# Optimization experiments

Hardware: AMD Instinct MI355X
Metric: run time of the kernel (lower is better)

The kernel has to match this reference:

```python
import jax, jax.numpy as jnp
import numpy as np

B, D_IN, D_LAT, K = 8192, 768, 12288, 64


def setup_inputs() -> dict:
    key = jax.random.key(0)
    k1, k2, k3 = jax.random.split(key, 3)
    x = jax.random.normal(k1, (B, D_IN), dtype=jnp.float32)
    # Kaiming-uniform-ish init scale (matches nn.Linear default magnitude)
    W_enc = jax.random.normal(k2, (D_IN, D_LAT), dtype=jnp.float32) * (1.0 / np.sqrt(D_IN))
    b_enc = jnp.zeros((D_LAT,), dtype=jnp.float32)
    W_dec = jax.random.normal(k3, (D_LAT, D_IN), dtype=jnp.float32) * (1.0 / np.sqrt(D_LAT))
    b_dec = jnp.zeros((D_IN,), dtype=jnp.float32)
    return {"x": x, "W_enc": W_enc, "b_enc": b_enc, "W_dec": W_dec, "b_dec": b_dec, "k_top": K}


def topk_activation(h, k):
    # keep top-k values per row, zero the rest (equivalent to zeros_like + scatter_)
    if k >= h.shape[1]:
        return h
    vals, idx = jax.lax.top_k(h, k)                  # [B, k]
    rows = jnp.arange(h.shape[0])[:, None]           # [B, 1]
    return jnp.zeros_like(h).at[rows, idx].set(vals)


def reference(x, W_enc, b_enc, W_dec, b_dec, k_top):
    h = x @ W_enc + b_enc                            # [B, D_LAT]
    z = topk_activation(h, k_top)                    # sparse latent [B, D_LAT]
    recon = z @ W_dec + b_dec                        # [B, D_IN]
    return recon, z
```

## Files before the change

### kernel.cpp

```cpp
#include <hip/hip_runtime.h>
#include <stdint.h>

#define BROWS 8192
#define DIN   768
#define DLAT  12288
#define KTOP  64

#define LO_SCALE 4096.0f
#define LO_INV   (1.0f / 4096.0f)


typedef _Float16 half8 __attribute__((ext_vector_type(8)));
typedef __attribute__((ext_vector_type(4))) float float4v;

typedef __attribute__((address_space(3))) void lds_void_t;
typedef __attribute__((address_space(1))) void glob_void_t;

__device__ __forceinline__ unsigned short f2h_bits(float f) {
  _Float16 h = (_Float16)f;
  return __builtin_bit_cast(unsigned short, h);
}
__device__ __forceinline__ float h_bits_to_f(unsigned short b) {
  return (float)__builtin_bit_cast(_Float16, b);
}

__global__ __launch_bounds__(256) void k_cvt_split(const float* __restrict__ in,
                                                   unsigned short* __restrict__ hi,
                                                   unsigned short* __restrict__ lo,
                                                   int n4) {
  int i = blockIdx.x * 256 + threadIdx.x;
  if (i >= n4) return;
  float4 v = ((const float4*)in)[i];
  ushort4 h, l;
  h.x = f2h_bits(v.x); l.x = f2h_bits((v.x - h_bits_to_f(h.x)) * LO_SCALE);
  h.y = f2h_bits(v.y); l.y = f2h_bits((v.y - h_bits_to_f(h.y)) * LO_SCALE);
  h.z = f2h_bits(v.z); l.z = f2h_bits((v.z - h_bits_to_f(h.z)) * LO_SCALE);
  h.w = f2h_bits(v.w); l.w = f2h_bits((v.w - h_bits_to_f(h.w)) * LO_SCALE);
  ((ushort4*)hi)[i] = h;
  ((ushort4*)lo)[i] = l;
}

__global__ __launch_bounds__(256) void k_transpose_split(const float* __restrict__ W,
                                                         unsigned short* __restrict__ Wth,
                                                         unsigned short* __restrict__ Wtl) {
  __shared__ float s[32][33];
  const int n0 = blockIdx.x * 32;
  const int k0 = blockIdx.y * 32;
  const int tx = threadIdx.x, ty = threadIdx.y;
#pragma unroll
  for (int i = 0; i < 4; i++)
    s[ty + 8 * i][tx] = W[(size_t)(k0 + ty + 8 * i) * DLAT + n0 + tx];
  __syncthreads();
#pragma unroll
  for (int i = 0; i < 4; i++) {
    int nl = ty + 8 * i;
    float v = s[tx][nl];
    unsigned short h = f2h_bits(v);
    unsigned short l = f2h_bits((v - h_bits_to_f(h)) * LO_SCALE);
    size_t o = (size_t)(n0 + nl) * DIN + k0 + tx;
    Wth[o] = h;
    Wtl[o] = l;
  }
}

#define GBM 256
#define GBN 128
#define GBK 32

#define MFMA12(MI, AH, AL)                                                                   \
  do {                                                                                       \
    _Pragma("unroll") for (int ni = 0; ni < 4; ni++) {                                       \
      acc1[MI][ni] = __builtin_amdgcn_mfma_f32_16x16x32_f16(AH, bh[ni], acc1[MI][ni], 0, 0, 0); \
      acc2[MI][ni] = __builtin_amdgcn_mfma_f32_16x16x32_f16(AL, bh[ni], acc2[MI][ni], 0, 0, 0); \
      acc2[MI][ni] = __builtin_amdgcn_mfma_f32_16x16x32_f16(AH, bl[ni], acc2[MI][ni], 0, 0, 0); \
    }                                                                                        \
  } while (0)

#define STAGE1(R)                                                                            \
  __builtin_amdgcn_global_load_lds((glob_void_t*)(src[R] + kk2),                             \
                                   (lds_void_t*)(sb + loff[R]), 16, 0, 0)

__global__ __launch_bounds__(512, 2) void k_enc_gemm(const unsigned short* __restrict__ Xh,
                                                     const unsigned short* __restrict__ Xl,
                                                     const unsigned short* __restrict__ Wth,
                                                     const unsigned short* __restrict__ Wtl,
                                                     const float* __restrict__ b_enc,
                                                     float* __restrict__ H) {
  __shared__ unsigned short lds[3][24576];

  const int tid  = threadIdx.x;
  const int lane = tid & 63;
  const int wave = tid >> 6;
  const int wm   = wave >> 1;
  const int wn   = wave & 1;

  const int wg = (blockIdx.x & 7) * 384 + (blockIdx.x >> 3);
  const int tm = wg / 96;
  const int tn = wg - tm * 96;
  const int m_blk = tm * GBM;
  const int n_blk = tn * GBN;

  const int qlog = (lane & 3) ^ ((lane >> 3) & 3);
  const unsigned short* src[6];
  int loff[6];
#pragma unroll
  for (int r = 0; r < 6; r++) {
    const int c = wave * 6 + r;
    const unsigned short* base;
    int grow;
    if (c < 16)      { base = Xh;  grow = m_blk + c * 16; }
    else if (c < 32) { base = Xl;  grow = m_blk + (c - 16) * 16; }
    else if (c < 40) { base = Wth; grow = n_blk + (c - 32) * 16; }
    else             { base = Wtl; grow = n_blk + (c - 40) * 16; }
    src[r]  = base + (size_t)(grow + (lane >> 2)) * DIN + qlog * 8;
    loff[r] = c * 512;
  }

  const int qp   = (lane >> 4) ^ ((lane >> 1) & 3);
  const int aoff = (wm * 64 + (lane & 15)) * 32 + qp * 8;
  const int boff = 16384 + (wn * 64 + (lane & 15)) * 32 + qp * 8;

  float4v acc1[4][4];
  float4v acc2[4][4];
#pragma unroll
  for (int i = 0; i < 4; i++)
#pragma unroll
    for (int j = 0; j < 4; j++) { acc1[i][j] = (float4v)0.0f; acc2[i][j] = (float4v)0.0f; }

#pragma unroll
  for (int r = 0; r < 6; r++)
    __builtin_amdgcn_global_load_lds((glob_void_t*)(src[r]),
                                     (lds_void_t*)(&lds[0][loff[r]]), 16, 0, 0);
#pragma unroll
  for (int r = 0; r < 6; r++)
    __builtin_amdgcn_global_load_lds((glob_void_t*)(src[r] + GBK),
                                     (lds_void_t*)(&lds[1][loff[r]]), 16, 0, 0);
  asm volatile("s_waitcnt vmcnt(6)" ::: "memory");
  asm volatile("s_barrier" ::: "memory");

  const unsigned short* p_cur = lds[0];
  const unsigned short* p_nxt = lds[1];
  unsigned short*       p_stg = lds[2];

#pragma unroll 1
  for (int t = 0; t < 24; t++) {
    const unsigned short* lb = p_cur;
    unsigned short*       sb = p_stg;
    const int kk2 = t * GBK + 2 * GBK;
    const bool do_stage = (t < 22);

    half8 bh[4], bl[4], ah0, al0, ah1, al1;

#pragma unroll
    for (int ni = 0; ni < 4; ni++) {
      bh[ni] = *(const half8*)(lb + boff + ni * 512);
      bl[ni] = *(const half8*)(lb + boff + 4096 + ni * 512);
    }
    ah0 = *(const half8*)(lb + aoff);
    al0 = *(const half8*)(lb + aoff + 8192);
    ah1 = *(const half8*)(lb + aoff + 512);
    al1 = *(const half8*)(lb + aoff + 8192 + 512);
    if (do_stage) { STAGE1(0); STAGE1(1); STAGE1(2); }
    __builtin_amdgcn_s_setprio(1);
    MFMA12(0, ah0, al0);
    MFMA12(1, ah1, al1);
    __builtin_amdgcn_s_setprio(0);

    ah0 = *(const half8*)(lb + aoff + 1024);
    al0 = *(const half8*)(lb + aoff + 8192 + 1024);
    ah1 = *(const half8*)(lb + aoff + 1536);
    al1 = *(const half8*)(lb + aoff + 8192 + 1536);
    if (do_stage) { STAGE1(3); STAGE1(4); STAGE1(5); }
    __builtin_amdgcn_s_setprio(1);
    MFMA12(2, ah0, al0);
    MFMA12(3, ah1, al1);
    __builtin_amdgcn_s_setprio(0);

    asm volatile("s_waitcnt lgkmcnt(0)" ::: "memory");
    if (t < 22)       { asm volatile("s_waitcnt vmcnt(6)" ::: "memory"); }
    else if (t == 22) { asm volatile("s_waitcnt vmcnt(0)" ::: "memory"); }
    asm volatile("s_barrier" ::: "memory");

    const unsigned short* tmp = p_cur;
    p_cur = p_nxt;
    p_nxt = p_stg;
    p_stg = (unsigned short*)tmp;
  }

  const int col   = lane & 15;
  const int rbase = (lane >> 4) * 4;
#pragma unroll
  for (int ni = 0; ni < 4; ni++) {
    const int n = n_blk + wn * 64 + ni * 16 + col;
    const float bias = b_enc[n];
#pragma unroll
    for (int mi = 0; mi < 4; mi++) {
#pragma unroll
      for (int r = 0; r < 4; r++) {
        const int m = m_blk + wm * 64 + mi * 16 + rbase + r;
        H[(size_t)m * DLAT + n] = acc1[mi][ni][r] + acc2[mi][ni][r] * LO_INV + bias;
      }
    }
  }
}

#define UMARGIN 4e-4f
#define UCAP 64
__device__ __forceinline__ float key_to_f32(unsigned k) {
  unsigned u = (k & 0x80000000u) ? (k & 0x7fffffffu) : ~k;
  return __uint_as_float(u);
}
#define KIDX(J) (4 * tid + 1024 * ((J) >> 2) + ((J) & 3))

__global__ __launch_bounds__(256) void k_topk(float* __restrict__ Z,
                                              const float* __restrict__ x,
                                              const float* __restrict__ We,
                                              const float* __restrict__ b_enc,
                                              int* __restrict__ idxl,
                                              float* __restrict__ vall) {
  const int row = blockIdx.x;
  const int tid = threadIdx.x;
  const int lane = tid & 63, wid = tid >> 6;
  float* zr = Z + (size_t)row * DLAT;

  unsigned keys[48];
#pragma unroll
  for (int j4 = 0; j4 < 12; j4++) {
    const float4 v4 = ((const float4*)zr)[tid + 256 * j4];
    const float vv[4] = {v4.x, v4.y, v4.z, v4.w};
#pragma unroll
    for (int c = 0; c < 4; c++) {
      const unsigned u = __float_as_uint(vv[c]);
      keys[4 * j4 + c] = (u & 0x80000000u) ? ~u : (u | 0x80000000u);
    }
  }

  __shared__ int hist[1024];
  __shared__ unsigned wmax[4];
  __shared__ unsigned s_kmax;
  __shared__ unsigned s_cur;
  __shared__ int wsum[4];
  __shared__ int s_total;
  __shared__ int s_krem;
  __shared__ int s_nu, s_ncert, s_out;
  __shared__ int   u_idx[UCAP];
  __shared__ float u_vf[UCAP];
  __shared__ unsigned char u_sel[UCAP];

  unsigned kmax = 0;
#pragma unroll
  for (int j = 0; j < 48; j++) kmax = max(kmax, keys[j]);
#pragma unroll
  for (int off = 32; off > 0; off >>= 1) {
    const unsigned tmp = (unsigned)__shfl_xor((int)kmax, off);
    kmax = max(kmax, tmp);
  }
  if (lane == 0) wmax[wid] = kmax;
  __syncthreads();
  if (tid == 0)
    s_kmax = max(max(wmax[0], wmax[1]), max(wmax[2], wmax[3]));
  __syncthreads();

  int b = (int)(s_kmax >> 24);
  int cum = 0;
  int bsel = 0, krem0 = KTOP;
#pragma unroll 1
  for (;;) {
    int c = 0;
#pragma unroll
    for (int j = 0; j < 48; j++) {
      const int by = (int)(keys[j] >> 24);
      c += (by == b) ? 0x10000 : 0;
      c += (by == b - 1) ? 1 : 0;
    }
#pragma unroll
    for (int off = 32; off > 0; off >>= 1) c += __shfl_down(c, off);
    if (lane == 0) wsum[wid] = c;
    __syncthreads();
    if (tid == 0) s_total = wsum[0] + wsum[1] + wsum[2] + wsum[3];
    __syncthreads();
    const int chi = s_total >> 16;
    const int clo = s_total & 0xffff;
    if (cum + chi >= KTOP) { bsel = b;     krem0 = KTOP - cum;        break; }
    if (cum + chi + clo >= KTOP) { bsel = b - 1; krem0 = KTOP - cum - chi; break; }
    cum += chi + clo;
    b -= 2;
    if (b < 0) { bsel = 0; krem0 = KTOP - cum; break; }
  }
  if (tid == 0) { s_cur = (unsigned)bsel << 24; s_krem = krem0; }
  __syncthreads();

#pragma unroll
  for (int r = 1; r < 4; r++) {
    const int sh = 24 - 8 * r;
    const unsigned pre = s_cur;
    hist[tid] = 0; hist[tid + 256] = 0; hist[tid + 512] = 0; hist[tid + 768] = 0;
    __syncthreads();
#pragma unroll
    for (int j = 0; j < 48; j++) {
      const unsigned k = keys[j];
      if ((((unsigned long long)(k ^ pre)) >> (sh + 8)) == 0ull)
        atomicAdd(&hist[wid * 256 + ((k >> sh) & 255)], 1);
    }
    __syncthreads();
    if (wid == 0) {
      const int b0 = 4 * lane;
      int t0 = hist[b0]     + hist[256 + b0]     + hist[512 + b0]     + hist[768 + b0];
      int t1 = hist[b0 + 1] + hist[256 + b0 + 1] + hist[512 + b0 + 1] + hist[768 + b0 + 1];
      int t2 = hist[b0 + 2] + hist[256 + b0 + 2] + hist[512 + b0 + 2] + hist[768 + b0 + 2];
      int t3 = hist[b0 + 3] + hist[256 + b0 + 3] + hist[512 + b0 + 3] + hist[768 + b0 + 3];
      const int s3 = t3, s2 = t2 + s3, s1 = t1 + s2, s0 = t0 + s1;
      int hi = s0;
#pragma unroll
      for (int off = 1; off < 64; off <<= 1) {
        const int tmp = __shfl_down(hi, off);
        if (lane + off < 64) hi += tmp;
      }
      const int krem = s_krem;
      const int S0 = hi, S1 = hi - s0 + s1, S2 = hi - s0 + s2, S3 = hi - s0 + s3;
      int bb = -1;
      if (S0 >= krem) bb = b0;
      if (S1 >= krem) bb = b0 + 1;
      if (S2 >= krem) bb = b0 + 2;
      if (S3 >= krem) bb = b0 + 3;
#pragma unroll
      for (int off = 1; off < 64; off <<= 1) bb = max(bb, __shfl_xor(bb, off));
      if ((bb >> 2) == lane) {
        const int c = bb & 3;
        const int Sb = (c == 0) ? S0 : (c == 1) ? S1 : (c == 2) ? S2 : S3;
        const int tc = (c == 0) ? t0 : (c == 1) ? t1 : (c == 2) ? t2 : t3;
        s_krem = krem - (Sb - tc);
        s_cur  = pre | ((unsigned)bb << sh);
      }
    }
    __syncthreads();
  }
  const unsigned cur = s_cur;
  const float h64 = key_to_f32(cur);

  if (tid == 0) { s_nu = 0; s_ncert = 0; s_out = 0; }
  __syncthreads();

  signed char uslot[48];
  int certc = 0;
#pragma unroll
  for (int j = 0; j < 48; j++) {
    const float v = key_to_f32(keys[j]);
    uslot[j] = -1;
    if (v > h64 + UMARGIN) {
      certc++;
    } else if (v >= h64 - UMARGIN) {
      int pos = atomicAdd(&s_nu, 1);
      if (pos < UCAP) {
        u_idx[pos] = KIDX(j);
        u_vf[pos]  = v;
        uslot[j] = (signed char)pos;
      }
    }
  }
  if (certc) atomicAdd(&s_ncert, certc);
  __syncthreads();

  const int nu = min(s_nu, UCAP);
  int t = KTOP - s_ncert;
  t = max(0, min(t, nu));

  if (nu > t) {
    if (tid < nu) {
      const int ci = u_idx[tid];
      const float* xr = x + (size_t)row * DIN;
      float c = 0.0f;
      for (int k = 0; k < DIN; k++)
        c = fmaf(xr[k], We[(size_t)k * DLAT + ci], c);
      u_vf[tid] = c + b_enc[ci];
    }
    __syncthreads();
    if (tid == 0) {
      for (int u = 0; u < nu; u++) {
        int rank = 0;
        for (int v2 = 0; v2 < nu; v2++)
          rank += (u_vf[v2] > u_vf[u]) ||
                  (u_vf[v2] == u_vf[u] && u_idx[v2] > u_idx[u]);
        u_sel[u] = (rank < t) ? 1 : 0;
      }
    }
  } else {
    if (tid < nu) u_sel[tid] = 1;
  }
  __syncthreads();

#pragma unroll
  for (int j4 = 0; j4 < 12; j4++) {
    float oc[4];
#pragma unroll
    for (int c = 0; c < 4; c++) {
      const int j = 4 * j4 + c;
      const int idx = 4 * tid + 1024 * j4 + c;
      const float v = key_to_f32(keys[j]);
      bool sel = false;
      float outv = 0.0f;
      if (v > h64 + UMARGIN) {
        sel = true; outv = v;
      } else if (uslot[j] >= 0 && u_sel[(int)uslot[j]]) {
        sel = true; outv = u_vf[(int)uslot[j]];
      }
      oc[c] = sel ? outv : 0.0f;
      if (sel) {
        int s = atomicAdd(&s_out, 1);
        if (s < KTOP) {
          idxl[row * KTOP + s] = idx;
          vall[row * KTOP + s] = outv;
        }
      }
    }
    float4 o;
    o.x = oc[0]; o.y = oc[1]; o.z = oc[2]; o.w = oc[3];
    ((float4*)zr)[tid + 256 * j4] = o;
  }
}

__global__ __launch_bounds__(192) void k_dec(const int* __restrict__ idxl,
                                             const float* __restrict__ vall,
                                             const float* __restrict__ Wd,
                                             const float* __restrict__ b_dec,
                                             float* __restrict__ R) {
  const int row = blockIdx.x;
  const int t = threadIdx.x;
  __shared__ int   sidx[KTOP];
  __shared__ float sval[KTOP];
  if (t < KTOP) {
    sidx[t] = idxl[row * KTOP + t];
    sval[t] = vall[row * KTOP + t];
  }
  __syncthreads();
  const int c = t * 4;
  float4 acc = *(const float4*)(b_dec + c);
#pragma unroll 4
  for (int j = 0; j < KTOP; j++) {
    float4 w = *(const float4*)(Wd + (size_t)sidx[j] * DIN + c);
    const float v = sval[j];
    acc.x += v * w.x;
    acc.y += v * w.y;
    acc.z += v * w.z;
    acc.w += v * w.w;
  }
  *(float4*)(R + (size_t)row * DIN + c) = acc;
}

extern "C" void kernel_launch(void* const* d_in, const int* in_sizes, int n_in,
                              void* d_out, int out_size, void* d_ws, size_t ws_size,
                              hipStream_t stream) {
  const float* x     = (const float*)d_in[0];
  const float* W_enc = (const float*)d_in[1];
  const float* b_enc = (const float*)d_in[2];
  const float* W_dec = (const float*)d_in[3];
  const float* b_dec = (const float*)d_in[4];

  float* recon = (float*)d_out;
  float* z     = (float*)d_out + (size_t)BROWS * DIN;

  unsigned short* Xh = (unsigned short*)recon;
  unsigned short* Xl = Xh + (size_t)BROWS * DIN;

  char* ws = (char*)d_ws;
  unsigned short* Wth = (unsigned short*)ws;
  unsigned short* Wtl = (unsigned short*)(ws + 18874368);
  int*   idxl = (int*)(ws + 2 * 18874368);
  float* vall = (float*)(ws + 2 * 18874368 + 2097152);

  k_cvt_split<<<6144, 256, 0, stream>>>(x, Xh, Xl, (BROWS * DIN) / 4);
  k_transpose_split<<<dim3(DLAT / 32, DIN / 32), dim3(32, 8), 0, stream>>>(W_enc, Wth, Wtl);
  k_enc_gemm<<<dim3(3072), dim3(512), 0, stream>>>(Xh, Xl, Wth, Wtl, b_enc, z);
  k_topk<<<BROWS, 256, 0, stream>>>(z, x, W_enc, b_enc, idxl, vall);
  k_dec<<<BROWS, 192, 0, stream>>>(idxl, vall, W_dec, b_dec, recon);
}
```

Measured before the change: 1.432 ms.

## Shrink encoder GEMM tile to 128x128 with 256 threads and double buffering

Halves the encoder GEMM M tile from 256 to 128 rows, uses 4 waves per block instead of 8, and launches twice as many workgroups. The LDS pipeline goes from three buffers with a prefetch depth of two to two buffers with a full vmcnt(0) wait every iteration. The aim is a smaller LDS footprint and more blocks per CU for latency hiding. In exchange each block reuses its loaded data less, and the loop exposes more global-load latency.

```diff
diff --git a/kernel.cpp b/kernel.cpp
--- a/kernel.cpp
+++ b/kernel.cpp
@@ -63,7 +63,7 @@
   }
 }
 
-#define GBM 256
+#define GBM 128
 #define GBN 128
 #define GBK 32
 
@@ -80,13 +80,13 @@
   __builtin_amdgcn_global_load_lds((glob_void_t*)(src[R] + kk2),                             \
                                    (lds_void_t*)(sb + loff[R]), 16, 0, 0)
 
-__global__ __launch_bounds__(512, 2) void k_enc_gemm(const unsigned short* __restrict__ Xh,
+__global__ __launch_bounds__(256, 2) void k_enc_gemm(const unsigned short* __restrict__ Xh,
                                                      const unsigned short* __restrict__ Xl,
                                                      const unsigned short* __restrict__ Wth,
                                                      const unsigned short* __restrict__ Wtl,
                                                      const float* __restrict__ b_enc,
                                                      float* __restrict__ H) {
-  __shared__ unsigned short lds[3][24576];
+  __shared__ unsigned short lds[2][16384];
 
   const int tid  = threadIdx.x;
   const int lane = tid & 63;
@@ -94,31 +94,32 @@
   const int wm   = wave >> 1;
   const int wn   = wave & 1;
 
-  const int wg = (blockIdx.x & 7) * 384 + (blockIdx.x >> 3);
+  const int wg = (blockIdx.x & 7) * 768 + (blockIdx.x >> 3);
   const int tm = wg / 96;
   const int tn = wg - tm * 96;
   const int m_blk = tm * GBM;
   const int n_blk = tn * GBN;
 
   const int qlog = (lane & 3) ^ ((lane >> 3) & 3);
-  const unsigned short* src[6];
-  int loff[6];
-#pragma unroll
-  for (int r = 0; r < 6; r++) {
-    const int c = wave * 6 + r;
+  const unsigned short* src[8];
+  int loff[8];
+#pragma unroll
+  for (int r = 0; r < 8; r++) {
+    const int c = wave * 8 + r;
+    const int k16 = (c & 7) * 16;
     const unsigned short* base;
     int grow;
-    if (c < 16)      { base = Xh;  grow = m_blk + c * 16; }
-    else if (c < 32) { base = Xl;  grow = m_blk + (c - 16) * 16; }
-    else if (c < 40) { base = Wth; grow = n_blk + (c - 32) * 16; }
-    else             { base = Wtl; grow = n_blk + (c - 40) * 16; }
+    if (c < 8)       { base = Xh;  grow = m_blk + k16; }
+    else if (c < 16) { base = Xl;  grow = m_blk + k16; }
+    else if (c < 24) { base = Wth; grow = n_blk + k16; }
+    else             { base = Wtl; grow = n_blk + k16; }
     src[r]  = base + (size_t)(grow + (lane >> 2)) * DIN + qlog * 8;
     loff[r] = c * 512;
   }
 
   const int qp   = (lane >> 4) ^ ((lane >> 1) & 3);
   const int aoff = (wm * 64 + (lane & 15)) * 32 + qp * 8;
-  const int boff = 16384 + (wn * 64 + (lane & 15)) * 32 + qp * 8;
+  const int boff = 8192 + (wn * 64 + (lane & 15)) * 32 + qp * 8;
 
   float4v acc1[4][4];
   float4v acc2[4][4];
@@ -128,26 +129,21 @@
     for (int j = 0; j < 4; j++) { acc1[i][j] = (float4v)0.0f; acc2[i][j] = (float4v)0.0f; }
 
 #pragma unroll
-  for (int r = 0; r < 6; r++)
+  for (int r = 0; r < 8; r++)
     __builtin_amdgcn_global_load_lds((glob_void_t*)(src[r]),
                                      (lds_void_t*)(&lds[0][loff[r]]), 16, 0, 0);
-#pragma unroll
-  for (int r = 0; r < 6; r++)
-    __builtin_amdgcn_global_load_lds((glob_void_t*)(src[r] + GBK),
-                                     (lds_void_t*)(&lds[1][loff[r]]), 16, 0, 0);
-  asm volatile("s_waitcnt vmcnt(6)" ::: "memory");
+  asm volatile("s_waitcnt vmcnt(0)" ::: "memory");
   asm volatile("s_barrier" ::: "memory");
 
   const unsigned short* p_cur = lds[0];
-  const unsigned short* p_nxt = lds[1];
-  unsigned short*       p_stg = lds[2];
+  unsigned short*       p_stg = lds[1];
 
 #pragma unroll 1
   for (int t = 0; t < 24; t++) {
     const unsigned short* lb = p_cur;
     unsigned short*       sb = p_stg;
-    const int kk2 = t * GBK + 2 * GBK;
-    const bool do_stage = (t < 22);
+    const int kk2 = t * GBK + GBK;
+    const bool do_stage = (t < 23);
 
     half8 bh[4], bl[4], ah0, al0, ah1, al1;
 
@@ -157,34 +153,31 @@
       bl[ni] = *(const half8*)(lb + boff + 4096 + ni * 512);
     }
     ah0 = *(const half8*)(lb + aoff);
-    al0 = *(const half8*)(lb + aoff + 8192);
+    al0 = *(const half8*)(lb + aoff + 4096);
     ah1 = *(const half8*)(lb + aoff + 512);
-    al1 = *(const half8*)(lb + aoff + 8192 + 512);
-    if (do_stage) { STAGE1(0); STAGE1(1); STAGE1(2); }
+    al1 = *(const half8*)(lb + aoff + 4096 + 512);
+    if (do_stage) { STAGE1(0); STAGE1(1); STAGE1(2); STAGE1(3); }
     __builtin_amdgcn_s_setprio(1);
     MFMA12(0, ah0, al0);
     MFMA12(1, ah1, al1);
     __builtin_amdgcn_s_setprio(0);
 
     ah0 = *(const half8*)(lb + aoff + 1024);
-    al0 = *(const half8*)(lb + aoff + 8192 + 1024);
+    al0 = *(const half8*)(lb + aoff + 4096 + 1024);
     ah1 = *(const half8*)(lb + aoff + 1536);
-    al1 = *(const half8*)(lb + aoff + 8192 + 1536);
-    if (do_stage) { STAGE1(3); STAGE1(4); STAGE1(5); }
+    al1 = *(const half8*)(lb + aoff + 4096 + 1536);
+    if (do_stage) { STAGE1(4); STAGE1(5); STAGE1(6); STAGE1(7); }
     __builtin_amdgcn_s_setprio(1);
     MFMA12(2, ah0, al0);
     MFMA12(3, ah1, al1);
     __builtin_amdgcn_s_setprio(0);
 
-    asm volatile("s_waitcnt lgkmcnt(0)" ::: "memory");
-    if (t < 22)       { asm volatile("s_waitcnt vmcnt(6)" ::: "memory"); }
-    else if (t == 22) { asm volatile("s_waitcnt vmcnt(0)" ::: "memory"); }
+    asm volatile("s_waitcnt vmcnt(0) lgkmcnt(0)" ::: "memory");
     asm volatile("s_barrier" ::: "memory");
 
-    const unsigned short* tmp = p_cur;
-    p_cur = p_nxt;
-    p_nxt = p_stg;
-    p_stg = (unsigned short*)tmp;
+    unsigned short* tmp = (unsigned short*)p_cur;
+    p_cur = p_stg;
+    p_stg = tmp;
   }
 
   const int col   = lane & 15;
@@ -470,7 +463,7 @@
 
   k_cvt_split<<<6144, 256, 0, stream>>>(x, Xh, Xl, (BROWS * DIN) / 4);
   k_transpose_split<<<dim3(DLAT / 32, DIN / 32), dim3(32, 8), 0, stream>>>(W_enc, Wth, Wtl);
-  k_enc_gemm<<<dim3(3072), dim3(512), 0, stream>>>(Xh, Xl, Wth, Wtl, b_enc, z);
+  k_enc_gemm<<<dim3(6144), dim3(256), 0, stream>>>(Xh, Xl, Wth, Wtl, b_enc, z);
   k_topk<<<BROWS, 256, 0, stream>>>(z, x, W_enc, b_enc, idxl, vall);
   k_dec<<<BROWS, 192, 0, stream>>>(idxl, vall, W_dec, b_dec, recon);
 }
```

New measurement: 1.458 ms. Within noise of the previous version (+1.9%).
